# Kernel optimization log

Hardware: AMD Instinct MI355X
Metric: run time of the kernel (lower is better)

Reference implementation:

```python
import jax, jax.numpy as jnp
import numpy as np

CHI = 24          # bond dimension (A0[0].shape[0])
K_PATHS = 16      # number of sampled spin strings
N_SPINS = 34      # N = 2**k + 2 with k = 5


def setup_inputs() -> dict:
    key = jax.random.key(0)
    k1, k2 = jax.random.split(key)
    # positive entries -> positive traces -> valid probabilities (stochastic MPS regime)
    A = jax.random.uniform(k1, (2, CHI, CHI), dtype=jnp.float32)
    samples = jax.random.randint(k2, (K_PATHS, N_SPINS), 0, 2).astype(jnp.int32)
    return {"A": A, "samples": samples}


def _kron(X, Y):
    d = X.shape[0] * Y.shape[0]
    return jnp.einsum('ij,kl->ikjl', X, Y).reshape(d, d)


def reference(A, samples):
    chi = A.shape[1]
    Au, Ad = A[0], A[1]
    AAu = _kron(Au, Au)              # [chi^2, chi^2]
    AAd = _kron(Ad, Ad)
    E = AAu + AAd                    # transfer matrix
    E2 = E @ E

    N = samples.shape[1]
    log2N = int(np.log2(N - 2))      # static: matches self.log2N
    E2k = E2
    for _ in range(log2N - 1):       # repeated squaring with trace normalization
        E2k = E2k @ E2k
        E2k = E2k / jnp.trace(E2k)
    EN = E2k @ E2                    # E^N up to overall scale

    def path_loglikelihood(spins):
        def step(String, s):
            Su = String @ AAu
            Sd = String @ AAd
            tr_u = jnp.trace(Su)
            tr_d = jnp.trace(Sd)
            tot = tr_u + tr_d
            p = jnp.where(s == 1, tr_u, tr_d) / tot
            # normalize by total trace: probabilities are scale-invariant ratios,
            # so this is mathematically identical but numerically stable
            String_new = jnp.where(s == 1, Su, Sd) / tot
            return String_new, jnp.log(p)

        _, logps = jax.lax.scan(step, EN, spins)
        return jnp.sum(logps)

    ll = jax.vmap(path_loglikelihood)(samples)   # [K_paths]
    return -jnp.sum(ll)                          # negative loglikelihood objective
```

## Files before the change

### kernel.cpp

```cpp
#include <hip/hip_runtime.h>
#include <math.h>


#define CHI     24
#define CHI2    576
#define NPATH   16
#define NSPIN   34
#define NT      512
#define PITERS  3
#define SCALE_P  0.00390625f
#define SCALE_Z  0.00390625f
#define SCALE_A  0.0625f
#define SCALE_A2 0.00390625f

#define LDS_FENCE() asm volatile("s_waitcnt lgkmcnt(0)" ::: "memory")

__device__ __forceinline__ int tb_of(int w) { return (w < 2) ? 5 * w : (4 * w + 2); }

__device__ __forceinline__ float hsum4(float4 a) { return (a.x + a.z) + (a.y + a.w); }
__device__ __forceinline__ void fma4(float4& acc, const float4 a, const float4 b) {
    acc.x = fmaf(a.x, b.x, acc.x);
    acc.y = fmaf(a.y, b.y, acc.y);
    acc.z = fmaf(a.z, b.z, acc.z);
    acc.w = fmaf(a.w, b.w, acc.w);
}

__device__ __forceinline__ void mm_tile(const float* __restrict__ X,
                                        const float* __restrict__ Y,
                                        int i0, int j0, float o[3][3]) {
    const float4* X0 = (const float4*)(X + (i0 + 0) * CHI);
    const float4* X1 = (const float4*)(X + (i0 + 1) * CHI);
    const float4* X2 = (const float4*)(X + (i0 + 2) * CHI);
    const float4* Y0 = (const float4*)(Y + (j0 + 0) * CHI);
    const float4* Y1 = (const float4*)(Y + (j0 + 1) * CHI);
    const float4* Y2 = (const float4*)(Y + (j0 + 2) * CHI);
    float4 acc[3][3];
    #pragma unroll
    for (int a = 0; a < 3; ++a)
        #pragma unroll
        for (int b = 0; b < 3; ++b) acc[a][b] = make_float4(0.f, 0.f, 0.f, 0.f);
    #pragma unroll
    for (int v = 0; v < 6; ++v) {
        const float4 x0 = X0[v], x1 = X1[v], x2 = X2[v];
        const float4 y0 = Y0[v], y1 = Y1[v], y2 = Y2[v];
        fma4(acc[0][0], x0, y0); fma4(acc[0][1], x0, y1); fma4(acc[0][2], x0, y2);
        fma4(acc[1][0], x1, y0); fma4(acc[1][1], x1, y1); fma4(acc[1][2], x1, y2);
        fma4(acc[2][0], x2, y0); fma4(acc[2][1], x2, y1); fma4(acc[2][2], x2, y2);
    }
    #pragma unroll
    for (int a = 0; a < 3; ++a)
        #pragma unroll
        for (int b = 0; b < 3; ++b) o[a][b] = hsum4(acc[a][b]);
}

__device__ __forceinline__ void mm_tile2(const float* __restrict__ Xa,
                                         const float* __restrict__ Xb,
                                         const float* __restrict__ Y,
                                         int i0, int j0, float o1[3][3], float o2[3][3]) {
    const float4* A0 = (const float4*)(Xa + (i0 + 0) * CHI);
    const float4* A1 = (const float4*)(Xa + (i0 + 1) * CHI);
    const float4* A2 = (const float4*)(Xa + (i0 + 2) * CHI);
    const float4* B0 = (const float4*)(Xb + (i0 + 0) * CHI);
    const float4* B1 = (const float4*)(Xb + (i0 + 1) * CHI);
    const float4* B2 = (const float4*)(Xb + (i0 + 2) * CHI);
    const float4* Y0 = (const float4*)(Y + (j0 + 0) * CHI);
    const float4* Y1 = (const float4*)(Y + (j0 + 1) * CHI);
    const float4* Y2 = (const float4*)(Y + (j0 + 2) * CHI);
    float4 p[3][3], q[3][3];
    #pragma unroll
    for (int a = 0; a < 3; ++a)
        #pragma unroll
        for (int b = 0; b < 3; ++b) {
            p[a][b] = make_float4(0.f, 0.f, 0.f, 0.f);
            q[a][b] = make_float4(0.f, 0.f, 0.f, 0.f);
        }
    #pragma unroll
    for (int v = 0; v < 6; ++v) {
        const float4 y0 = Y0[v], y1 = Y1[v], y2 = Y2[v];
        const float4 a0 = A0[v], a1 = A1[v], a2 = A2[v];
        fma4(p[0][0], a0, y0); fma4(p[0][1], a0, y1); fma4(p[0][2], a0, y2);
        fma4(p[1][0], a1, y0); fma4(p[1][1], a1, y1); fma4(p[1][2], a1, y2);
        fma4(p[2][0], a2, y0); fma4(p[2][1], a2, y1); fma4(p[2][2], a2, y2);
        const float4 b0 = B0[v], b1 = B1[v], b2 = B2[v];
        fma4(q[0][0], b0, y0); fma4(q[0][1], b0, y1); fma4(q[0][2], b0, y2);
        fma4(q[1][0], b1, y0); fma4(q[1][1], b1, y1); fma4(q[1][2], b1, y2);
        fma4(q[2][0], b2, y0); fma4(q[2][1], b2, y1); fma4(q[2][2], b2, y2);
    }
    #pragma unroll
    for (int a = 0; a < 3; ++a)
        #pragma unroll
        for (int b = 0; b < 3; ++b) { o1[a][b] = hsum4(p[a][b]); o2[a][b] = hsum4(q[a][b]); }
}

__device__ __forceinline__ void mm_tile_dual(const float* __restrict__ X1,
                                             const float* __restrict__ Y1,
                                             const float* __restrict__ X2,
                                             const float* __restrict__ Y2,
                                             int i0, int j0, float o1[3][3], float o2[3][3]) {
    const float4* A0 = (const float4*)(X1 + (i0 + 0) * CHI);
    const float4* A1 = (const float4*)(X1 + (i0 + 1) * CHI);
    const float4* A2 = (const float4*)(X1 + (i0 + 2) * CHI);
    const float4* U0 = (const float4*)(Y1 + (j0 + 0) * CHI);
    const float4* U1 = (const float4*)(Y1 + (j0 + 1) * CHI);
    const float4* U2 = (const float4*)(Y1 + (j0 + 2) * CHI);
    const float4* B0 = (const float4*)(X2 + (i0 + 0) * CHI);
    const float4* B1 = (const float4*)(X2 + (i0 + 1) * CHI);
    const float4* B2 = (const float4*)(X2 + (i0 + 2) * CHI);
    const float4* V0 = (const float4*)(Y2 + (j0 + 0) * CHI);
    const float4* V1 = (const float4*)(Y2 + (j0 + 1) * CHI);
    const float4* V2 = (const float4*)(Y2 + (j0 + 2) * CHI);
    float4 p[3][3], q[3][3];
    #pragma unroll
    for (int a = 0; a < 3; ++a)
        #pragma unroll
        for (int b = 0; b < 3; ++b) {
            p[a][b] = make_float4(0.f, 0.f, 0.f, 0.f);
            q[a][b] = make_float4(0.f, 0.f, 0.f, 0.f);
        }
    #pragma unroll
    for (int v = 0; v < 6; ++v) {
        const float4 a0 = A0[v], a1 = A1[v], a2 = A2[v];
        const float4 u0 = U0[v], u1 = U1[v], u2 = U2[v];
        fma4(p[0][0], a0, u0); fma4(p[0][1], a0, u1); fma4(p[0][2], a0, u2);
        fma4(p[1][0], a1, u0); fma4(p[1][1], a1, u1); fma4(p[1][2], a1, u2);
        fma4(p[2][0], a2, u0); fma4(p[2][1], a2, u1); fma4(p[2][2], a2, u2);
        const float4 b0 = B0[v], b1 = B1[v], b2 = B2[v];
        const float4 w0 = V0[v], w1 = V1[v], w2 = V2[v];
        fma4(q[0][0], b0, w0); fma4(q[0][1], b0, w1); fma4(q[0][2], b0, w2);
        fma4(q[1][0], b1, w0); fma4(q[1][1], b1, w1); fma4(q[1][2], b1, w2);
        fma4(q[2][0], b2, w0); fma4(q[2][1], b2, w1); fma4(q[2][2], b2, w2);
    }
    #pragma unroll
    for (int a = 0; a < 3; ++a)
        #pragma unroll
        for (int b = 0; b < 3; ++b) { o1[a][b] = hsum4(p[a][b]); o2[a][b] = hsum4(q[a][b]); }
}

__device__ __forceinline__ void st_tile(float* __restrict__ D, int i0, int j0,
                                        const float o[3][3], float s) {
    #pragma unroll
    for (int a = 0; a < 3; ++a)
        #pragma unroll
        for (int b = 0; b < 3; ++b) D[(i0 + a) * CHI + j0 + b] = o[a][b] * s;
}
__device__ __forceinline__ void st_tileT(float* __restrict__ D, int i0, int j0,
                                         const float o[3][3], float s) {
    #pragma unroll
    for (int a = 0; a < 3; ++a)
        #pragma unroll
        for (int b = 0; b < 3; ++b) D[(j0 + b) * CHI + i0 + a] = o[a][b] * s;
}

__global__ __launch_bounds__(NT) void mps_ll_kernel(
    const float* __restrict__ A,
    const int*   __restrict__ samples,
    float*       __restrict__ out,
    float*       __restrict__ ws)
{
    __shared__ alignas(16) float sAu[CHI2], sAd[CHI2], sAuT[CHI2], sAdT[CHI2];
    __shared__ alignas(16) float sL[CHI2], sR[CHI2], sGu[CHI2], sGd[CHI2];
    __shared__ alignas(16) float bO1[CHI2], bO2[CHI2], bQ1[CHI2], bQ2[CHI2];
    __shared__ alignas(16) float wsG[8][CHI2];
    __shared__ alignas(16) float wsGT[8][CHI2];
    __shared__ alignas(16) float wsP[8][CHI2];
    __shared__ alignas(16) float wsPT[8][CHI2];
    __shared__ float llw[8];
    __shared__ int   doneCnt;

    const int tid  = threadIdx.x;
    const int w    = tid >> 6;
    const int lane = tid & 63;
    const int path = blockIdx.x;
    const int i0 = 3 * (lane >> 3), j0 = 3 * (lane & 7);

    if (tid == 0) doneCnt = 0;
    for (int k = tid; k < CHI2; k += NT) {
        const int r = k / CHI, c = k % CHI;
        const float u = A[k], d = A[CHI2 + k];
        sAu[k] = u; sAd[k] = d;
        sAuT[c * CHI + r] = u; sAdT[c * CHI + r] = d;
        sR[k] = 1.0f; sL[k] = 1.0f;
    }
    const int sp = (lane < NSPIN) ? samples[path * NSPIN + lane] : 0;
    const unsigned long long smask = __ballot(sp != 0);
    __syncthreads();

    if (w == 0) {
        float o1[3][3], o2[3][3];
        for (int it = 0; it <= PITERS; ++it) {
            mm_tile2(sAu, sAd, sR, i0, j0, o1, o2);
            LDS_FENCE();
            st_tile(bO1, i0, j0, o1, 1.0f);
            st_tile(bO2, i0, j0, o2, 1.0f);
            LDS_FENCE();
            mm_tile_dual(bO1, sAu, bO2, sAd, i0, j0, o1, o2);
            LDS_FENCE();
            if (it < PITERS) {
                #pragma unroll
                for (int a = 0; a < 3; ++a)
                    #pragma unroll
                    for (int b = 0; b < 3; ++b)
                        sR[(i0 + a) * CHI + j0 + b] = (o1[a][b] + o2[a][b]) * SCALE_P;
            } else {
                st_tile(sGu, i0, j0, o1, SCALE_P);
                st_tile(sGd, i0, j0, o2, SCALE_P);
            }
            LDS_FENCE();
        }
    } else if (w == 4) {
        float o1[3][3], o2[3][3];
        for (int it = 0; it < PITERS; ++it) {
            mm_tile2(sAuT, sAdT, sL, i0, j0, o1, o2);
            LDS_FENCE();
            st_tile(bQ1, i0, j0, o1, 1.0f);
            st_tile(bQ2, i0, j0, o2, 1.0f);
            LDS_FENCE();
            mm_tile_dual(bQ1, sAuT, bQ2, sAdT, i0, j0, o1, o2);
            LDS_FENCE();
            #pragma unroll
            for (int a = 0; a < 3; ++a)
                #pragma unroll
                for (int b = 0; b < 3; ++b)
                    sL[(i0 + a) * CHI + j0 + b] = (o1[a][b] + o2[a][b]) * SCALE_P;
            LDS_FENCE();
        }
    } else {
        int g0 = -1, g1 = -1;
        if      (w == 1) g0 = 0;
        else if (w == 2) g0 = 1;
        else if (w == 3) g0 = 2;
        else if (w == 5) g0 = 3;
        else if (w == 6) g0 = 4;
        else             { g0 = 5; g1 = 6; }
        for (int gi = 0; gi < 2; ++gi) {
            const int g = (gi == 0) ? g0 : g1;
            if (g < 0) break;
            const int e0 = tb_of(g), e1 = tb_of(g + 1);
            float o[3][3];
            const float* X = ((smask >> e0) & 1ULL) ? sAu : sAd;
            const float* Y = ((smask >> (e0 + 1)) & 1ULL) ? sAuT : sAdT;
            mm_tile(X, Y, i0, j0, o);
            LDS_FENCE();
            st_tile(wsG[g], i0, j0, o, SCALE_A2);
            LDS_FENCE();
            float ls = SCALE_A2;
            for (int e = e0 + 2; e < e1; ++e) {
                const float* AT = ((smask >> e) & 1ULL) ? sAuT : sAdT;
                mm_tile(wsG[g], AT, i0, j0, o);
                LDS_FENCE();
                st_tile(wsG[g], i0, j0, o, SCALE_A);
                LDS_FENCE();
                ls = SCALE_A;
            }
            st_tileT(wsGT[g], i0, j0, o, ls);
            LDS_FENCE();
        }
        if (lane == 0)
            __hip_atomic_fetch_add(&doneCnt, 1, __ATOMIC_RELEASE, __HIP_MEMORY_SCOPE_WORKGROUP);
        if (w == 1) {
            while (__hip_atomic_load(&doneCnt, __ATOMIC_ACQUIRE, __HIP_MEMORY_SCOPE_WORKGROUP) < 6)
                __builtin_amdgcn_s_sleep(2);
            const float* prow = wsG[0];
            for (int j = 2; j <= 7; ++j) {
                float o[3][3];
                mm_tile(prow, wsGT[j - 1], i0, j0, o);
                LDS_FENCE();
                st_tile(wsP[j], i0, j0, o, 1.0f);
                st_tileT(wsPT[j], i0, j0, o, 1.0f);
                LDS_FENCE();
                prow = wsP[j];
            }
        }
    }
    __syncthreads();

    float gu[3][3], gd[3][3], zt[3][3];
    #pragma unroll
    for (int a = 0; a < 3; ++a)
        #pragma unroll
        for (int b = 0; b < 3; ++b) {
            gu[a][b] = sGu[(i0 + a) * CHI + j0 + b];
            gd[a][b] = sGd[(i0 + a) * CHI + j0 + b];
        }
    float* zbuf = wsP[w];
    float* pbuf = wsG[w];
    if (w == 0) {
        for (int k = lane; k < CHI2; k += 64) zbuf[k] = sL[k];
        #pragma unroll
        for (int a = 0; a < 3; ++a)
            #pragma unroll
            for (int b = 0; b < 3; ++b) zt[a][b] = sL[(i0 + a) * CHI + j0 + b];
        LDS_FENCE();
    } else {
        const float* ET = (w == 1) ? wsGT[0] : wsPT[w];
        float n[3][3];
        mm_tile(sL, ET, i0, j0, n);
        LDS_FENCE();
        st_tileT(pbuf, i0, j0, n, 1.0f);
        LDS_FENCE();
        mm_tile(ET, pbuf, i0, j0, zt);
        LDS_FENCE();
        st_tile(zbuf, i0, j0, zt, 1.0f);
        LDS_FENCE();
    }

    const int ta = tb_of(w), te = tb_of(w + 1);
    float ll = 0.0f;
    for (int t = ta; t < te; ++t) {
        float pu = 0.f, pd = 0.f;
        #pragma unroll
        for (int a = 0; a < 3; ++a)
            #pragma unroll
            for (int b = 0; b < 3; ++b) {
                pu = fmaf(zt[a][b], gu[a][b], pu);
                pd = fmaf(zt[a][b], gd[a][b], pd);
            }
        const int bit = (int)((smask >> t) & 1ULL);
        const bool more = (t + 1 < te);
        const float* AT = bit ? sAuT : sAdT;
        if (more) {
            float p[3][3];
            mm_tile(AT, zbuf, i0, j0, p);
            LDS_FENCE();
            st_tile(pbuf, i0, j0, p, 1.0f);
        }
        #pragma unroll
        for (int off = 1; off < 64; off <<= 1) {
            pu += __shfl_xor(pu, off);
            pd += __shfl_xor(pd, off);
        }
        ll += __logf(bit ? pu : pd) - __logf(pu + pd);
        if (more) {
            LDS_FENCE();
            float zn[3][3];
            mm_tile(pbuf, AT, i0, j0, zn);
            LDS_FENCE();
            #pragma unroll
            for (int a = 0; a < 3; ++a)
                #pragma unroll
                for (int b = 0; b < 3; ++b) zt[a][b] = zn[a][b] * SCALE_Z;
            st_tile(zbuf, i0, j0, zt, 1.0f);
            LDS_FENCE();
        }
    }

    if (lane == 0) llw[w] = ll;
    __syncthreads();

    if (tid == 0) {
        float s = 0.f;
        #pragma unroll
        for (int i = 0; i < 8; ++i) s += llw[i];
        unsigned* wsu = (unsigned*)ws;
        __hip_atomic_store(&ws[16 + path], s, __ATOMIC_RELAXED, __HIP_MEMORY_SCOPE_AGENT);
        const unsigned old = __hip_atomic_fetch_add(&wsu[0], 1u, __ATOMIC_ACQ_REL,
                                                    __HIP_MEMORY_SCOPE_AGENT);
        if (old == 0xAAAAAAAAu + (unsigned)(NPATH - 1) || old == (unsigned)(NPATH - 1)) {
            float tot = 0.f;
            #pragma unroll
            for (int i = 0; i < NPATH; ++i)
                tot += __hip_atomic_load(&ws[16 + i], __ATOMIC_RELAXED,
                                         __HIP_MEMORY_SCOPE_AGENT);
            out[0] = -tot;
        }
    }
}

extern "C" void kernel_launch(void* const* d_in, const int* in_sizes, int n_in,
                              void* d_out, int out_size, void* d_ws, size_t ws_size,
                              hipStream_t stream) {
    const float* A       = (const float*)d_in[0];
    const int*   samples = (const int*)d_in[1];
    float*       out     = (float*)d_out;
    float*       ws      = (float*)d_ws;

    mps_ll_kernel<<<NPATH, NT, 0, stream>>>(A, samples, out, ws);
}
```

Before: 78.04 us.

## Replace serial prefix chain with tree schedule and fine-grained wave flags

Replaces the single-wave serial prefix-product chain with a three-wave tree computation coordinated by LDS flags and counters. It also removes the block-wide barrier so each wave starts its scan segment as soon as its own inputs are ready. The segment boundaries are rebalanced, the power iteration for the right environment drops one step, and the inner scan keeps A rows in registers across both half-products. The final cross-block reduction now uses a wave shuffle. This adds more spin-wait synchronisation and LDS use. Cutting one power iteration may also change numerical accuracy.

```diff
diff --git a/kernel.cpp b/kernel.cpp
--- a/kernel.cpp
+++ b/kernel.cpp
@@ -2,12 +2,13 @@
 #include <math.h>
 
 
-#define CHI     24
-#define CHI2    576
-#define NPATH   16
-#define NSPIN   34
-#define NT      512
-#define PITERS  3
+#define CHI      24
+#define CHI2     576
+#define NPATH    16
+#define NSPIN    34
+#define NT       512
+#define PITERS_R 2
+#define PITERS_L 3
 #define SCALE_P  0.00390625f
 #define SCALE_Z  0.00390625f
 #define SCALE_A  0.0625f
@@ -15,7 +16,7 @@
 
 #define LDS_FENCE() asm volatile("s_waitcnt lgkmcnt(0)" ::: "memory")
 
-__device__ __forceinline__ int tb_of(int w) { return (w < 2) ? 5 * w : (4 * w + 2); }
+__device__ __forceinline__ int B_of(int i) { return 4 * i + (i > 0) + (i > 6); }
 
 __device__ __forceinline__ float hsum4(float4 a) { return (a.x + a.z) + (a.y + a.w); }
 __device__ __forceinline__ void fma4(float4& acc, const float4 a, const float4 b) {
@@ -151,6 +152,23 @@
         for (int b = 0; b < 3; ++b) D[(j0 + b) * CHI + i0 + a] = o[a][b] * s;
 }
 
+__device__ __forceinline__ void flag_set(int* f, int lane) {
+    LDS_FENCE();
+    if (lane == 0) __hip_atomic_store(f, 1, __ATOMIC_RELEASE, __HIP_MEMORY_SCOPE_WORKGROUP);
+}
+__device__ __forceinline__ void flag_wait(int* f) {
+    while (__hip_atomic_load(f, __ATOMIC_ACQUIRE, __HIP_MEMORY_SCOPE_WORKGROUP) == 0)
+        __builtin_amdgcn_s_sleep(1);
+}
+__device__ __forceinline__ void cnt_arrive(int* c, int lane) {
+    LDS_FENCE();
+    if (lane == 0) __hip_atomic_fetch_add(c, 1, __ATOMIC_ACQ_REL, __HIP_MEMORY_SCOPE_WORKGROUP);
+}
+__device__ __forceinline__ void cnt_wait(int* c, int n) {
+    while (__hip_atomic_load(c, __ATOMIC_ACQUIRE, __HIP_MEMORY_SCOPE_WORKGROUP) < n)
+        __builtin_amdgcn_s_sleep(1);
+}
+
 __global__ __launch_bounds__(NT) void mps_ll_kernel(
     const float* __restrict__ A,
     const int*   __restrict__ samples,
@@ -160,12 +178,13 @@
     __shared__ alignas(16) float sAu[CHI2], sAd[CHI2], sAuT[CHI2], sAdT[CHI2];
     __shared__ alignas(16) float sL[CHI2], sR[CHI2], sGu[CHI2], sGd[CHI2];
     __shared__ alignas(16) float bO1[CHI2], bO2[CHI2], bQ1[CHI2], bQ2[CHI2];
-    __shared__ alignas(16) float wsG[8][CHI2];
-    __shared__ alignas(16) float wsGT[8][CHI2];
-    __shared__ alignas(16) float wsP[8][CHI2];
+    __shared__ alignas(16) float wsC[7][CHI2], wsCT[7][CHI2];
     __shared__ alignas(16) float wsPT[8][CHI2];
+    __shared__ alignas(16) float treeR[3][CHI2];
+    __shared__ alignas(16) float treeT[3][CHI2];
+    __shared__ alignas(16) float wsZ[8][CHI2], wsS[8][CHI2];
     __shared__ float llw[8];
-    __shared__ int   doneCnt;
+    __shared__ int sFlag[24];
 
     const int tid  = threadIdx.x;
     const int w    = tid >> 6;
@@ -173,7 +192,7 @@
     const int path = blockIdx.x;
     const int i0 = 3 * (lane >> 3), j0 = 3 * (lane & 7);
 
-    if (tid == 0) doneCnt = 0;
+    if (tid < 24) sFlag[tid] = 0;
     for (int k = tid; k < CHI2; k += NT) {
         const int r = k / CHI, c = k % CHI;
         const float u = A[k], d = A[CHI2 + k];
@@ -187,7 +206,7 @@
 
     if (w == 0) {
         float o1[3][3], o2[3][3];
-        for (int it = 0; it <= PITERS; ++it) {
+        for (int it = 0; it <= PITERS_R; ++it) {
             mm_tile2(sAu, sAd, sR, i0, j0, o1, o2);
             LDS_FENCE();
             st_tile(bO1, i0, j0, o1, 1.0f);
@@ -195,21 +214,22 @@
             LDS_FENCE();
             mm_tile_dual(bO1, sAu, bO2, sAd, i0, j0, o1, o2);
             LDS_FENCE();
-            if (it < PITERS) {
+            if (it < PITERS_R) {
                 #pragma unroll
                 for (int a = 0; a < 3; ++a)
                     #pragma unroll
                     for (int b = 0; b < 3; ++b)
                         sR[(i0 + a) * CHI + j0 + b] = (o1[a][b] + o2[a][b]) * SCALE_P;
+                LDS_FENCE();
             } else {
                 st_tile(sGu, i0, j0, o1, SCALE_P);
                 st_tile(sGd, i0, j0, o2, SCALE_P);
-            }
-            LDS_FENCE();
+                flag_set(&sFlag[19], lane);
+            }
         }
     } else if (w == 4) {
         float o1[3][3], o2[3][3];
-        for (int it = 0; it < PITERS; ++it) {
+        for (int it = 0; it < PITERS_L; ++it) {
             mm_tile2(sAuT, sAdT, sL, i0, j0, o1, o2);
             LDS_FENCE();
             st_tile(bQ1, i0, j0, o1, 1.0f);
@@ -224,8 +244,9 @@
                     sL[(i0 + a) * CHI + j0 + b] = (o1[a][b] + o2[a][b]) * SCALE_P;
             LDS_FENCE();
         }
+        flag_set(&sFlag[18], lane);
     } else {
-        int g0 = -1, g1 = -1;
+        int g0, g1 = -1;
         if      (w == 1) g0 = 0;
         else if (w == 2) g0 = 1;
         else if (w == 3) g0 = 2;
@@ -235,55 +256,82 @@
         for (int gi = 0; gi < 2; ++gi) {
             const int g = (gi == 0) ? g0 : g1;
             if (g < 0) break;
-            const int e0 = tb_of(g), e1 = tb_of(g + 1);
+            const int e0 = B_of(g), e1 = B_of(g + 1);
             float o[3][3];
             const float* X = ((smask >> e0) & 1ULL) ? sAu : sAd;
             const float* Y = ((smask >> (e0 + 1)) & 1ULL) ? sAuT : sAdT;
             mm_tile(X, Y, i0, j0, o);
-            LDS_FENCE();
-            st_tile(wsG[g], i0, j0, o, SCALE_A2);
+            st_tile(wsC[g], i0, j0, o, SCALE_A2);
             LDS_FENCE();
             float ls = SCALE_A2;
             for (int e = e0 + 2; e < e1; ++e) {
                 const float* AT = ((smask >> e) & 1ULL) ? sAuT : sAdT;
-                mm_tile(wsG[g], AT, i0, j0, o);
+                mm_tile(wsC[g], AT, i0, j0, o);
                 LDS_FENCE();
-                st_tile(wsG[g], i0, j0, o, SCALE_A);
+                st_tile(wsC[g], i0, j0, o, SCALE_A);
                 LDS_FENCE();
                 ls = SCALE_A;
             }
-            st_tileT(wsGT[g], i0, j0, o, ls);
-            LDS_FENCE();
-        }
-        if (lane == 0)
-            __hip_atomic_fetch_add(&doneCnt, 1, __ATOMIC_RELEASE, __HIP_MEMORY_SCOPE_WORKGROUP);
-        if (w == 1) {
-            while (__hip_atomic_load(&doneCnt, __ATOMIC_ACQUIRE, __HIP_MEMORY_SCOPE_WORKGROUP) < 6)
-                __builtin_amdgcn_s_sleep(2);
-            const float* prow = wsG[0];
-            for (int j = 2; j <= 7; ++j) {
-                float o[3][3];
-                mm_tile(prow, wsGT[j - 1], i0, j0, o);
-                LDS_FENCE();
-                st_tile(wsP[j], i0, j0, o, 1.0f);
-                st_tileT(wsPT[j], i0, j0, o, 1.0f);
-                LDS_FENCE();
-                prow = wsP[j];
-            }
-        }
-    }
-    __syncthreads();
-
-    float gu[3][3], gd[3][3], zt[3][3];
-    #pragma unroll
-    for (int a = 0; a < 3; ++a)
-        #pragma unroll
-        for (int b = 0; b < 3; ++b) {
-            gu[a][b] = sGu[(i0 + a) * CHI + j0 + b];
-            gd[a][b] = sGd[(i0 + a) * CHI + j0 + b];
-        }
-    float* zbuf = wsP[w];
-    float* pbuf = wsG[w];
+            st_tileT(wsCT[g], i0, j0, o, ls);
+            flag_set(&sFlag[g], lane);
+        }
+        if (w == 2) {
+            float o[3][3];
+            flag_wait(&sFlag[0]);
+            mm_tile(wsC[0], wsCT[1], i0, j0, o);
+            LDS_FENCE();
+            st_tile(treeR[0], i0, j0, o, 1.0f);
+            st_tileT(wsPT[2], i0, j0, o, 1.0f);
+            cnt_arrive(&sFlag[16], lane); cnt_wait(&sFlag[16], 3);
+            mm_tile(treeR[0], treeT[0], i0, j0, o);
+            LDS_FENCE();
+            st_tile(treeR[2], i0, j0, o, 1.0f);
+            st_tileT(wsPT[4], i0, j0, o, 1.0f);
+            flag_set(&sFlag[8 + 4], lane);
+            cnt_arrive(&sFlag[17], lane); cnt_wait(&sFlag[17], 3);
+            mm_tile(treeR[2], treeT[1], i0, j0, o);
+            LDS_FENCE();
+            st_tileT(wsPT[6], i0, j0, o, 1.0f);
+            flag_set(&sFlag[8 + 6], lane);
+        } else if (w == 3) {
+            float o[3][3];
+            flag_wait(&sFlag[3]);
+            mm_tile(wsC[2], wsCT[3], i0, j0, o);
+            LDS_FENCE();
+            st_tileT(treeT[0], i0, j0, o, 1.0f);
+            cnt_arrive(&sFlag[16], lane); cnt_wait(&sFlag[16], 3);
+            mm_tile(treeR[0], wsCT[2], i0, j0, o);
+            LDS_FENCE();
+            st_tileT(wsPT[3], i0, j0, o, 1.0f);
+            cnt_arrive(&sFlag[17], lane); cnt_wait(&sFlag[17], 3);
+            mm_tile(treeR[2], wsCT[4], i0, j0, o);
+            LDS_FENCE();
+            st_tileT(wsPT[5], i0, j0, o, 1.0f);
+            flag_set(&sFlag[8 + 5], lane);
+        } else if (w == 5) {
+            float o[3][3];
+            flag_wait(&sFlag[4]); flag_wait(&sFlag[5]);
+            mm_tile(wsC[4], wsCT[5], i0, j0, o);
+            LDS_FENCE();
+            st_tile(treeR[1], i0, j0, o, 1.0f);
+            st_tileT(treeT[1], i0, j0, o, 1.0f);
+            cnt_arrive(&sFlag[16], lane); cnt_wait(&sFlag[16], 3);
+            flag_wait(&sFlag[6]);
+            mm_tile(treeR[1], wsCT[6], i0, j0, o);
+            LDS_FENCE();
+            st_tileT(treeT[2], i0, j0, o, 1.0f);
+            cnt_arrive(&sFlag[17], lane); cnt_wait(&sFlag[17], 3);
+            mm_tile(treeR[2], treeT[2], i0, j0, o);
+            LDS_FENCE();
+            st_tileT(wsPT[7], i0, j0, o, 1.0f);
+            flag_set(&sFlag[8 + 7], lane);
+        }
+    }
+
+    if (w != 4) flag_wait(&sFlag[18]);
+    float zt[3][3];
+    float* zbuf = wsZ[w];
+    float* pbuf = wsS[w];
     if (w == 0) {
         for (int k = lane; k < CHI2; k += 64) zbuf[k] = sL[k];
         #pragma unroll
@@ -292,7 +340,8 @@
             for (int b = 0; b < 3; ++b) zt[a][b] = sL[(i0 + a) * CHI + j0 + b];
         LDS_FENCE();
     } else {
-        const float* ET = (w == 1) ? wsGT[0] : wsPT[w];
+        if (w >= 4) flag_wait(&sFlag[8 + w]);
+        const float* ET = (w == 1) ? wsCT[0] : wsPT[w];
         float n[3][3];
         mm_tile(sL, ET, i0, j0, n);
         LDS_FENCE();
@@ -303,8 +352,17 @@
         st_tile(zbuf, i0, j0, zt, 1.0f);
         LDS_FENCE();
     }
-
-    const int ta = tb_of(w), te = tb_of(w + 1);
+    if (w != 0) flag_wait(&sFlag[19]);
+    float gu[3][3], gd[3][3];
+    #pragma unroll
+    for (int a = 0; a < 3; ++a)
+        #pragma unroll
+        for (int b = 0; b < 3; ++b) {
+            gu[a][b] = sGu[(i0 + a) * CHI + j0 + b];
+            gd[a][b] = sGd[(i0 + a) * CHI + j0 + b];
+        }
+
+    const int ta = B_of(w), te = B_of(w + 1);
     float ll = 0.0f;
     for (int t = ta; t < te; ++t) {
         float pu = 0.f, pd = 0.f;
@@ -317,12 +375,30 @@
             }
         const int bit = (int)((smask >> t) & 1ULL);
         const bool more = (t + 1 < te);
-        const float* AT = bit ? sAuT : sAdT;
+        float4 atr[3][6];
         if (more) {
-            float p[3][3];
-            mm_tile(AT, zbuf, i0, j0, p);
-            LDS_FENCE();
-            st_tile(pbuf, i0, j0, p, 1.0f);
+            const float* AT = bit ? sAuT : sAdT;
+            #pragma unroll
+            for (int a = 0; a < 3; ++a) {
+                const float4* r = (const float4*)(AT + (i0 + a) * CHI);
+                #pragma unroll
+                for (int v = 0; v < 6; ++v) atr[a][v] = r[v];
+            }
+            #pragma unroll
+            for (int jr = 0; jr < 3; ++jr) {
+                const float4* zr = (const float4*)(zbuf + (j0 + jr) * CHI);
+                float4 a0 = {0,0,0,0}, a1 = {0,0,0,0}, a2 = {0,0,0,0};
+                #pragma unroll
+                for (int v = 0; v < 6; ++v) {
+                    const float4 z = zr[v];
+                    fma4(a0, atr[0][v], z);
+                    fma4(a1, atr[1][v], z);
+                    fma4(a2, atr[2][v], z);
+                }
+                pbuf[(i0 + 0) * CHI + j0 + jr] = hsum4(a0);
+                pbuf[(i0 + 1) * CHI + j0 + jr] = hsum4(a1);
+                pbuf[(i0 + 2) * CHI + j0 + jr] = hsum4(a2);
+            }
         }
         #pragma unroll
         for (int off = 1; off < 64; off <<= 1) {
@@ -332,14 +408,25 @@
         ll += __logf(bit ? pu : pd) - __logf(pu + pd);
         if (more) {
             LDS_FENCE();
-            float zn[3][3];
-            mm_tile(pbuf, AT, i0, j0, zn);
-            LDS_FENCE();
-            #pragma unroll
-            for (int a = 0; a < 3; ++a)
+            #pragma unroll
+            for (int b = 0; b < 3; ++b) {
+                const float4* pr = (const float4*)(pbuf + (j0 + b) * CHI);
+                float4 a0 = {0,0,0,0}, a1 = {0,0,0,0}, a2 = {0,0,0,0};
                 #pragma unroll
-                for (int b = 0; b < 3; ++b) zt[a][b] = zn[a][b] * SCALE_Z;
-            st_tile(zbuf, i0, j0, zt, 1.0f);
+                for (int v = 0; v < 6; ++v) {
+                    const float4 p = pr[v];
+                    fma4(a0, p, atr[0][v]);
+                    fma4(a1, p, atr[1][v]);
+                    fma4(a2, p, atr[2][v]);
+                }
+                const float v0 = hsum4(a0) * SCALE_Z;
+                const float v1 = hsum4(a1) * SCALE_Z;
+                const float v2 = hsum4(a2) * SCALE_Z;
+                zbuf[(j0 + b) * CHI + i0 + 0] = v0;
+                zbuf[(j0 + b) * CHI + i0 + 1] = v1;
+                zbuf[(j0 + b) * CHI + i0 + 2] = v2;
+                zt[0][b] = v0; zt[1][b] = v1; zt[2][b] = v2;
+            }
             LDS_FENCE();
         }
     }
@@ -347,21 +434,27 @@
     if (lane == 0) llw[w] = ll;
     __syncthreads();
 
-    if (tid == 0) {
-        float s = 0.f;
-        #pragma unroll
-        for (int i = 0; i < 8; ++i) s += llw[i];
-        unsigned* wsu = (unsigned*)ws;
-        __hip_atomic_store(&ws[16 + path], s, __ATOMIC_RELAXED, __HIP_MEMORY_SCOPE_AGENT);
-        const unsigned old = __hip_atomic_fetch_add(&wsu[0], 1u, __ATOMIC_ACQ_REL,
-                                                    __HIP_MEMORY_SCOPE_AGENT);
-        if (old == 0xAAAAAAAAu + (unsigned)(NPATH - 1) || old == (unsigned)(NPATH - 1)) {
-            float tot = 0.f;
-            #pragma unroll
-            for (int i = 0; i < NPATH; ++i)
-                tot += __hip_atomic_load(&ws[16 + i], __ATOMIC_RELAXED,
-                                         __HIP_MEMORY_SCOPE_AGENT);
-            out[0] = -tot;
+    if (w == 0) {
+        int last = 0;
+        if (lane == 0) {
+            float s = 0.f;
+            #pragma unroll
+            for (int i = 0; i < 8; ++i) s += llw[i];
+            __hip_atomic_store(&ws[16 + path], s, __ATOMIC_RELAXED, __HIP_MEMORY_SCOPE_AGENT);
+            unsigned* wsu = (unsigned*)ws;
+            const unsigned old = __hip_atomic_fetch_add(&wsu[0], 1u, __ATOMIC_ACQ_REL,
+                                                        __HIP_MEMORY_SCOPE_AGENT);
+            last = (old == 0xAAAAAAAAu + (unsigned)(NPATH - 1) ||
+                    old == (unsigned)(NPATH - 1)) ? 1 : 0;
+        }
+        last = __shfl(last, 0);
+        if (last) {
+            float v = (lane < NPATH)
+                ? __hip_atomic_load(&ws[16 + lane], __ATOMIC_RELAXED, __HIP_MEMORY_SCOPE_AGENT)
+                : 0.f;
+            #pragma unroll
+            for (int off = 1; off < 16; off <<= 1) v += __shfl_xor(v, off);
+            if (lane == 0) out[0] = -v;
         }
     }
 }
```

New measurement: 84.50 us. 8.3% more time.

## Rebalance time-segment split, defer trace reductions, shorten power iterations

Applied to the files above, without the earlier changes.

Changes the segment boundaries assigned to each wave (B_of replaces tb_of) so the right and left power-iteration waves do fewer squaring rounds and the other waves carry a rebalanced share of segments. The per-step trace reductions are no longer interleaved with the matrix updates: each wave first records up to five Z snapshots in registers, then computes all traces and does one batched shuffle reduction. Also adds a launch_bounds occupancy hint, drops a redundant fence, and parallelizes the final cross-block sum with wave shuffles. This raises register pressure from holding snapshots, and changes the algebraic partition, which could affect numerical equivalence if the boundaries or iteration counts do not match the original math.

```diff
diff --git a/kernel.cpp b/kernel.cpp
--- a/kernel.cpp
+++ b/kernel.cpp
@@ -2,12 +2,13 @@
 #include <math.h>
 
 
-#define CHI     24
-#define CHI2    576
-#define NPATH   16
-#define NSPIN   34
-#define NT      512
-#define PITERS  3
+#define CHI      24
+#define CHI2     576
+#define NPATH    16
+#define NSPIN    34
+#define NT       512
+#define PITERS_R 2
+#define PITERS_L 2
 #define SCALE_P  0.00390625f
 #define SCALE_Z  0.00390625f
 #define SCALE_A  0.0625f
@@ -15,7 +16,9 @@
 
 #define LDS_FENCE() asm volatile("s_waitcnt lgkmcnt(0)" ::: "memory")
 
-__device__ __forceinline__ int tb_of(int w) { return (w < 2) ? 5 * w : (4 * w + 2); }
+__device__ __forceinline__ int B_of(int i) {
+    return 5 * i - 2 * ((i >= 2) + (i >= 7) + (i >= 8));
+}
 
 __device__ __forceinline__ float hsum4(float4 a) { return (a.x + a.z) + (a.y + a.w); }
 __device__ __forceinline__ void fma4(float4& acc, const float4 a, const float4 b) {
@@ -151,7 +154,7 @@
         for (int b = 0; b < 3; ++b) D[(j0 + b) * CHI + i0 + a] = o[a][b] * s;
 }
 
-__global__ __launch_bounds__(NT) void mps_ll_kernel(
+__global__ __launch_bounds__(NT, 2) void mps_ll_kernel(
     const float* __restrict__ A,
     const int*   __restrict__ samples,
     float*       __restrict__ out,
@@ -160,10 +163,9 @@
     __shared__ alignas(16) float sAu[CHI2], sAd[CHI2], sAuT[CHI2], sAdT[CHI2];
     __shared__ alignas(16) float sL[CHI2], sR[CHI2], sGu[CHI2], sGd[CHI2];
     __shared__ alignas(16) float bO1[CHI2], bO2[CHI2], bQ1[CHI2], bQ2[CHI2];
-    __shared__ alignas(16) float wsG[8][CHI2];
-    __shared__ alignas(16) float wsGT[8][CHI2];
-    __shared__ alignas(16) float wsP[8][CHI2];
-    __shared__ alignas(16) float wsPT[8][CHI2];
+    __shared__ alignas(16) float wsC[7][CHI2], wsCT[7][CHI2];
+    __shared__ alignas(16) float wsP[7][CHI2], wsPT[8][CHI2];
+    __shared__ alignas(16) float wsZ[8][CHI2], wsS[8][CHI2];
     __shared__ float llw[8];
     __shared__ int   doneCnt;
 
@@ -187,7 +189,7 @@
 
     if (w == 0) {
         float o1[3][3], o2[3][3];
-        for (int it = 0; it <= PITERS; ++it) {
+        for (int it = 0; it <= PITERS_R; ++it) {
             mm_tile2(sAu, sAd, sR, i0, j0, o1, o2);
             LDS_FENCE();
             st_tile(bO1, i0, j0, o1, 1.0f);
@@ -195,7 +197,7 @@
             LDS_FENCE();
             mm_tile_dual(bO1, sAu, bO2, sAd, i0, j0, o1, o2);
             LDS_FENCE();
-            if (it < PITERS) {
+            if (it < PITERS_R) {
                 #pragma unroll
                 for (int a = 0; a < 3; ++a)
                     #pragma unroll
@@ -209,7 +211,7 @@
         }
     } else if (w == 4) {
         float o1[3][3], o2[3][3];
-        for (int it = 0; it < PITERS; ++it) {
+        for (int it = 0; it < PITERS_L; ++it) {
             mm_tile2(sAuT, sAdT, sL, i0, j0, o1, o2);
             LDS_FENCE();
             st_tile(bQ1, i0, j0, o1, 1.0f);
@@ -225,7 +227,7 @@
             LDS_FENCE();
         }
     } else {
-        int g0 = -1, g1 = -1;
+        int g0, g1 = -1;
         if      (w == 1) g0 = 0;
         else if (w == 2) g0 = 1;
         else if (w == 3) g0 = 2;
@@ -235,55 +237,47 @@
         for (int gi = 0; gi < 2; ++gi) {
             const int g = (gi == 0) ? g0 : g1;
             if (g < 0) break;
-            const int e0 = tb_of(g), e1 = tb_of(g + 1);
+            const int e0 = B_of(g), e1 = B_of(g + 1);
             float o[3][3];
             const float* X = ((smask >> e0) & 1ULL) ? sAu : sAd;
             const float* Y = ((smask >> (e0 + 1)) & 1ULL) ? sAuT : sAdT;
             mm_tile(X, Y, i0, j0, o);
-            LDS_FENCE();
-            st_tile(wsG[g], i0, j0, o, SCALE_A2);
+            st_tile(wsC[g], i0, j0, o, SCALE_A2);
             LDS_FENCE();
             float ls = SCALE_A2;
             for (int e = e0 + 2; e < e1; ++e) {
                 const float* AT = ((smask >> e) & 1ULL) ? sAuT : sAdT;
-                mm_tile(wsG[g], AT, i0, j0, o);
-                LDS_FENCE();
-                st_tile(wsG[g], i0, j0, o, SCALE_A);
+                mm_tile(wsC[g], AT, i0, j0, o);
+                LDS_FENCE();
+                st_tile(wsC[g], i0, j0, o, SCALE_A);
                 LDS_FENCE();
                 ls = SCALE_A;
             }
-            st_tileT(wsGT[g], i0, j0, o, ls);
-            LDS_FENCE();
-        }
-        if (lane == 0)
+            st_tileT(wsCT[g], i0, j0, o, ls);
+            LDS_FENCE();
+        }
+        if (w != 1 && lane == 0)
             __hip_atomic_fetch_add(&doneCnt, 1, __ATOMIC_RELEASE, __HIP_MEMORY_SCOPE_WORKGROUP);
         if (w == 1) {
-            while (__hip_atomic_load(&doneCnt, __ATOMIC_ACQUIRE, __HIP_MEMORY_SCOPE_WORKGROUP) < 6)
+            while (__hip_atomic_load(&doneCnt, __ATOMIC_ACQUIRE, __HIP_MEMORY_SCOPE_WORKGROUP) < 5)
                 __builtin_amdgcn_s_sleep(2);
-            const float* prow = wsG[0];
+            const float* prow = wsC[0];
             for (int j = 2; j <= 7; ++j) {
                 float o[3][3];
-                mm_tile(prow, wsGT[j - 1], i0, j0, o);
-                LDS_FENCE();
-                st_tile(wsP[j], i0, j0, o, 1.0f);
+                mm_tile(prow, wsCT[j - 1], i0, j0, o);
+                LDS_FENCE();
+                st_tile(wsP[j - 1], i0, j0, o, 1.0f);
                 st_tileT(wsPT[j], i0, j0, o, 1.0f);
                 LDS_FENCE();
-                prow = wsP[j];
+                prow = wsP[j - 1];
             }
         }
     }
     __syncthreads();
 
-    float gu[3][3], gd[3][3], zt[3][3];
-    #pragma unroll
-    for (int a = 0; a < 3; ++a)
-        #pragma unroll
-        for (int b = 0; b < 3; ++b) {
-            gu[a][b] = sGu[(i0 + a) * CHI + j0 + b];
-            gd[a][b] = sGd[(i0 + a) * CHI + j0 + b];
-        }
-    float* zbuf = wsP[w];
-    float* pbuf = wsG[w];
+    float zt[3][3];
+    float* zbuf = wsZ[w];
+    float* pbuf = wsS[w];
     if (w == 0) {
         for (int k = lane; k < CHI2; k += 64) zbuf[k] = sL[k];
         #pragma unroll
@@ -292,7 +286,7 @@
             for (int b = 0; b < 3; ++b) zt[a][b] = sL[(i0 + a) * CHI + j0 + b];
         LDS_FENCE();
     } else {
-        const float* ET = (w == 1) ? wsGT[0] : wsPT[w];
+        const float* ET = (w == 1) ? wsCT[0] : wsPT[w];
         float n[3][3];
         mm_tile(sL, ET, i0, j0, n);
         LDS_FENCE();
@@ -304,64 +298,100 @@
         LDS_FENCE();
     }
 
-    const int ta = tb_of(w), te = tb_of(w + 1);
-    float ll = 0.0f;
-    for (int t = ta; t < te; ++t) {
-        float pu = 0.f, pd = 0.f;
-        #pragma unroll
-        for (int a = 0; a < 3; ++a)
-            #pragma unroll
-            for (int b = 0; b < 3; ++b) {
-                pu = fmaf(zt[a][b], gu[a][b], pu);
-                pd = fmaf(zt[a][b], gd[a][b], pd);
-            }
-        const int bit = (int)((smask >> t) & 1ULL);
-        const bool more = (t + 1 < te);
-        const float* AT = bit ? sAuT : sAdT;
-        if (more) {
-            float p[3][3];
-            mm_tile(AT, zbuf, i0, j0, p);
-            LDS_FENCE();
-            st_tile(pbuf, i0, j0, p, 1.0f);
-        }
-        #pragma unroll
-        for (int off = 1; off < 64; off <<= 1) {
-            pu += __shfl_xor(pu, off);
-            pd += __shfl_xor(pd, off);
-        }
-        ll += __logf(bit ? pu : pd) - __logf(pu + pd);
-        if (more) {
-            LDS_FENCE();
-            float zn[3][3];
-            mm_tile(pbuf, AT, i0, j0, zn);
-            LDS_FENCE();
+    const int ta = B_of(w), len = B_of(w + 1) - ta;
+    float zh[5][3][3];
+    #pragma unroll
+    for (int s = 0; s < 5; ++s) {
+        if (s < len) {
             #pragma unroll
             for (int a = 0; a < 3; ++a)
                 #pragma unroll
-                for (int b = 0; b < 3; ++b) zt[a][b] = zn[a][b] * SCALE_Z;
-            st_tile(zbuf, i0, j0, zt, 1.0f);
-            LDS_FENCE();
+                for (int b = 0; b < 3; ++b) zh[s][a][b] = zt[a][b];
+            if (s + 1 < len) {
+                const int bit = (int)((smask >> (ta + s)) & 1ULL);
+                const float* AT = bit ? sAuT : sAdT;
+                float p[3][3];
+                mm_tile(AT, zbuf, i0, j0, p);
+                LDS_FENCE();
+                st_tile(pbuf, i0, j0, p, 1.0f);
+                LDS_FENCE();
+                float zn[3][3];
+                mm_tile(pbuf, AT, i0, j0, zn);
+                LDS_FENCE();
+                #pragma unroll
+                for (int a = 0; a < 3; ++a)
+                    #pragma unroll
+                    for (int b = 0; b < 3; ++b) zt[a][b] = zn[a][b] * SCALE_Z;
+                st_tile(zbuf, i0, j0, zt, 1.0f);
+                LDS_FENCE();
+            }
+        }
+    }
+
+    float gu[3][3], gd[3][3];
+    #pragma unroll
+    for (int a = 0; a < 3; ++a)
+        #pragma unroll
+        for (int b = 0; b < 3; ++b) {
+            gu[a][b] = sGu[(i0 + a) * CHI + j0 + b];
+            gd[a][b] = sGd[(i0 + a) * CHI + j0 + b];
+        }
+    float pu5[5], pd5[5];
+    #pragma unroll
+    for (int s = 0; s < 5; ++s) {
+        float pu = 0.f, pd = 0.f;
+        if (s < len) {
+            #pragma unroll
+            for (int a = 0; a < 3; ++a)
+                #pragma unroll
+                for (int b = 0; b < 3; ++b) {
+                    pu = fmaf(zh[s][a][b], gu[a][b], pu);
+                    pd = fmaf(zh[s][a][b], gd[a][b], pd);
+                }
+        }
+        pu5[s] = pu; pd5[s] = pd;
+    }
+    #pragma unroll
+    for (int off = 1; off < 64; off <<= 1) {
+        #pragma unroll
+        for (int s = 0; s < 5; ++s) {
+            pu5[s] += __shfl_xor(pu5[s], off);
+            pd5[s] += __shfl_xor(pd5[s], off);
+        }
+    }
+    float ll = 0.f;
+    #pragma unroll
+    for (int s = 0; s < 5; ++s) {
+        if (s < len) {
+            const int bit = (int)((smask >> (ta + s)) & 1ULL);
+            ll += __logf(bit ? pu5[s] : pd5[s]) - __logf(pu5[s] + pd5[s]);
         }
     }
 
     if (lane == 0) llw[w] = ll;
     __syncthreads();
 
-    if (tid == 0) {
-        float s = 0.f;
-        #pragma unroll
-        for (int i = 0; i < 8; ++i) s += llw[i];
-        unsigned* wsu = (unsigned*)ws;
-        __hip_atomic_store(&ws[16 + path], s, __ATOMIC_RELAXED, __HIP_MEMORY_SCOPE_AGENT);
-        const unsigned old = __hip_atomic_fetch_add(&wsu[0], 1u, __ATOMIC_ACQ_REL,
-                                                    __HIP_MEMORY_SCOPE_AGENT);
-        if (old == 0xAAAAAAAAu + (unsigned)(NPATH - 1) || old == (unsigned)(NPATH - 1)) {
-            float tot = 0.f;
-            #pragma unroll
-            for (int i = 0; i < NPATH; ++i)
-                tot += __hip_atomic_load(&ws[16 + i], __ATOMIC_RELAXED,
-                                         __HIP_MEMORY_SCOPE_AGENT);
-            out[0] = -tot;
+    if (w == 0) {
+        int last = 0;
+        if (lane == 0) {
+            float s = 0.f;
+            #pragma unroll
+            for (int i = 0; i < 8; ++i) s += llw[i];
+            __hip_atomic_store(&ws[16 + path], s, __ATOMIC_RELAXED, __HIP_MEMORY_SCOPE_AGENT);
+            unsigned* wsu = (unsigned*)ws;
+            const unsigned old = __hip_atomic_fetch_add(&wsu[0], 1u, __ATOMIC_ACQ_REL,
+                                                        __HIP_MEMORY_SCOPE_AGENT);
+            last = (old == 0xAAAAAAAAu + (unsigned)(NPATH - 1) ||
+                    old == (unsigned)(NPATH - 1)) ? 1 : 0;
+        }
+        last = __shfl(last, 0);
+        if (last) {
+            float v = (lane < NPATH)
+                ? __hip_atomic_load(&ws[16 + lane], __ATOMIC_RELAXED, __HIP_MEMORY_SCOPE_AGENT)
+                : 0.f;
+            #pragma unroll
+            for (int off = 1; off < 16; off <<= 1) v += __shfl_xor(v, off);
+            if (lane == 0) out[0] = -v;
         }
     }
 }
```

Measured after the change: 81.58 us. 4.5% more time.
